# Performance work log

Hardware: AMD Instinct MI355X
Metric: run time of the kernel (lower is better)

The kernel has to match this reference:

```python
import jax, jax.numpy as jnp
import numpy as np

INPUT_DIM = 1024
HIDDEN_DIM = 1024


def setup_inputs() -> dict:
    key = jax.random.key(0)
    ks = jax.random.split(key, 7)
    B, S = 4, 2048
    s = 1.0 / np.sqrt(INPUT_DIM)
    x = jax.random.normal(ks[0], (B, S, INPUT_DIM), dtype=jnp.float32)
    Wq = jax.random.normal(ks[1], (HIDDEN_DIM, INPUT_DIM), dtype=jnp.float32) * s
    bq = jnp.zeros((HIDDEN_DIM,), dtype=jnp.float32)
    Wk = jax.random.normal(ks[2], (HIDDEN_DIM, INPUT_DIM), dtype=jnp.float32) * s
    bk = jnp.zeros((HIDDEN_DIM,), dtype=jnp.float32)
    Wv = jax.random.normal(ks[3], (HIDDEN_DIM, INPUT_DIM), dtype=jnp.float32) * s
    bv = jnp.zeros((HIDDEN_DIM,), dtype=jnp.float32)
    return {"x": x, "Wq": Wq, "bq": bq, "Wk": Wk, "bk": bk, "Wv": Wv, "bv": bv}


def reference(x, Wq, bq, Wk, bk, Wv, bv):
    # Linear layers: y = x @ W.T + b (torch nn.Linear convention)
    q = jnp.einsum('bsi,hi->bsh', x, Wq) + bq
    k = jnp.einsum('bsi,hi->bsh', x, Wk) + bk
    v = jnp.einsum('bsi,hi->bsh', x, Wv) + bv
    scale = 1.0 / jnp.sqrt(jnp.asarray(q.shape[-1], dtype=q.dtype))
    scores = jnp.einsum('bsh,bth->bst', q, k) * scale  # [B,S,S]
    attention_weights = jax.nn.softmax(scores, axis=-1)
    weighted_sum = jnp.einsum('bst,bth->bsh', attention_weights, v)
    return (weighted_sum, attention_weights)
```

## Files before the change

### kernel.cpp

```cpp
#include <hip/hip_runtime.h>
#include <hip/hip_bf16.h>
#include <cstdint>


typedef __bf16 bf16x8 __attribute__((ext_vector_type(8)));
typedef float  f32x4  __attribute__((ext_vector_type(4)));

__device__ __forceinline__ void load_lds16(const __bf16* g, __bf16* l) {
    __builtin_amdgcn_global_load_lds(
        (const __attribute__((address_space(1))) void*)g,
        (__attribute__((address_space(3))) void*)l,
        16, 0, 0);
}

__global__ __launch_bounds__(256) void cvt_f32_bf16(
        const float* __restrict__ src, __bf16* __restrict__ dst, int n8) {
    int i = blockIdx.x * blockDim.x + threadIdx.x;
    if (i >= n8) return;
    const float4* s4 = (const float4*)src;
    float4 a = s4[2 * i], b = s4[2 * i + 1];
    bf16x8 o;
    o[0] = (__bf16)a.x; o[1] = (__bf16)a.y; o[2] = (__bf16)a.z; o[3] = (__bf16)a.w;
    o[4] = (__bf16)b.x; o[5] = (__bf16)b.y; o[6] = (__bf16)b.z; o[7] = (__bf16)b.w;
    ((bf16x8*)dst)[i] = o;
}

__global__ __launch_bounds__(256) void pack_bias3(
        const float* __restrict__ a, const float* __restrict__ b,
        const float* __restrict__ c, float* __restrict__ o) {
    int i = blockIdx.x * blockDim.x + threadIdx.x;
    if (i < 1024) { o[i] = a[i]; o[i + 1024] = b[i]; o[i + 2048] = c[i]; }
}

template <int MODE>
__global__ __launch_bounds__(256, 3) void gemm_nt(
        const __bf16* __restrict__ A, const __bf16* __restrict__ Bt,
        void* __restrict__ C0, void* __restrict__ C1, void* __restrict__ C2,
        const float* __restrict__ bias,
        int lda, int ldb, int ldc, long sA, long sB, long sC,
        int K, float scale) {
    __shared__ __bf16 lA[128 * 64];
    __shared__ __bf16 lB[128 * 64];

    const int tid  = threadIdx.x;
    const int lane = tid & 63;
    const int wave = tid >> 6;
    const int mblk = blockIdx.y * 128;
    const int nblk = blockIdx.x * 128;
    const int z    = blockIdx.z;
    A  += (long)z * sA;
    Bt += (long)z * sB;

    const int wm = (wave >> 1) * 64;
    const int wn = (wave & 1) * 64;

    f32x4 zero = {0.f, 0.f, 0.f, 0.f};
    f32x4 acc[4][4];
#pragma unroll
    for (int i = 0; i < 4; ++i)
#pragma unroll
        for (int j = 0; j < 4; ++j) acc[i][j] = zero;

    const int rsel = lane & 15;
    const int quad = lane >> 4;

    int srow[4], scol[4];
#pragma unroll
    for (int it = 0; it < 4; ++it) {
        int s  = tid + it * 256;
        srow[it] = s >> 3;
        scol[it] = ((s & 7) ^ (srow[it] & 7)) * 8;
    }

    for (int k0 = 0; k0 < K; k0 += 64) {
#pragma unroll
        for (int it = 0; it < 4; ++it) {
            int s = tid + it * 256;
            load_lds16(A  + (long)(mblk + srow[it]) * lda + k0 + scol[it], lA + s * 8);
            load_lds16(Bt + (long)(nblk + srow[it]) * ldb + k0 + scol[it], lB + s * 8);
        }
        __syncthreads();

#pragma unroll
        for (int half = 0; half < 2; ++half) {
            const int cq = quad + half * 4;
            bf16x8 fa[4], fb[4];
#pragma unroll
            for (int i = 0; i < 4; ++i) {
                int ra = wm + i * 16 + rsel;
                fa[i] = *(const bf16x8*)&lA[(ra * 8 + (cq ^ (ra & 7))) * 8];
                int rb = wn + i * 16 + rsel;
                fb[i] = *(const bf16x8*)&lB[(rb * 8 + (cq ^ (rb & 7))) * 8];
            }
#pragma unroll
            for (int i = 0; i < 4; ++i)
#pragma unroll
                for (int j = 0; j < 4; ++j)
                    acc[i][j] = __builtin_amdgcn_mfma_f32_16x16x32_bf16(
                        fa[i], fb[j], acc[i][j], 0, 0, 0);
        }
        __syncthreads();
    }

    const int rq = quad * 4;
#pragma unroll
    for (int i = 0; i < 4; ++i) {
#pragma unroll
        for (int j = 0; j < 4; ++j) {
            const int n = nblk + wn + j * 16 + rsel;
            if constexpr (MODE == 0) {
                __bf16* C = (n < 1024) ? (__bf16*)C0
                          : (n < 2048) ? (__bf16*)C1 : (__bf16*)C2;
                const int col = n & 1023;
                float bv = bias[n];
#pragma unroll
                for (int r = 0; r < 4; ++r) {
                    int m = mblk + wm + i * 16 + rq + r;
                    C[(long)m * ldc + col] = (__bf16)(acc[i][j][r] + bv);
                }
            } else if constexpr (MODE == 1) {
                float* C = (float*)C0 + (long)z * sC;
#pragma unroll
                for (int r = 0; r < 4; ++r) {
                    int m = mblk + wm + i * 16 + rq + r;
                    C[(long)m * ldc + n] = acc[i][j][r] * scale;
                }
            } else {
                float* C = (float*)C0 + (long)z * sC;
#pragma unroll
                for (int r = 0; r < 4; ++r) {
                    int m = mblk + wm + i * 16 + rq + r;
                    C[(long)m * ldc + n] = acc[i][j][r];
                }
            }
        }
    }
}

__global__ __launch_bounds__(256) void softmax_rows(
        float* __restrict__ P, __bf16* __restrict__ Pb) {
    const long row = blockIdx.x;
    float*  p  = P  + row * 2048;
    __bf16* pb = Pb + row * 2048;
    const int tid  = threadIdx.x;
    const int lane = tid & 63;
    const int wave = tid >> 6;

    float4 v0 = ((const float4*)p)[tid * 2];
    float4 v1 = ((const float4*)p)[tid * 2 + 1];
    float e[8] = {v0.x, v0.y, v0.z, v0.w, v1.x, v1.y, v1.z, v1.w};

    float mx = e[0];
#pragma unroll
    for (int i = 1; i < 8; ++i) mx = fmaxf(mx, e[i]);
#pragma unroll
    for (int o = 1; o < 64; o <<= 1) mx = fmaxf(mx, __shfl_xor(mx, o, 64));

    __shared__ float redm[4], reds[4];
    if (lane == 0) redm[wave] = mx;
    __syncthreads();
    mx = fmaxf(fmaxf(redm[0], redm[1]), fmaxf(redm[2], redm[3]));

    float sum = 0.f;
#pragma unroll
    for (int i = 0; i < 8; ++i) { e[i] = __expf(e[i] - mx); sum += e[i]; }
#pragma unroll
    for (int o = 1; o < 64; o <<= 1) sum += __shfl_xor(sum, o, 64);
    if (lane == 0) reds[wave] = sum;
    __syncthreads();
    sum = reds[0] + reds[1] + reds[2] + reds[3];
    const float inv = 1.f / sum;

    float4 o0, o1;
    o0.x = e[0] * inv; o0.y = e[1] * inv; o0.z = e[2] * inv; o0.w = e[3] * inv;
    o1.x = e[4] * inv; o1.y = e[5] * inv; o1.z = e[6] * inv; o1.w = e[7] * inv;
    ((float4*)p)[tid * 2]     = o0;
    ((float4*)p)[tid * 2 + 1] = o1;
    bf16x8 ob;
    ob[0] = (__bf16)o0.x; ob[1] = (__bf16)o0.y; ob[2] = (__bf16)o0.z; ob[3] = (__bf16)o0.w;
    ob[4] = (__bf16)o1.x; ob[5] = (__bf16)o1.y; ob[6] = (__bf16)o1.z; ob[7] = (__bf16)o1.w;
    ((bf16x8*)pb)[tid] = ob;
}

__global__ __launch_bounds__(256) void transpose_v(
        const __bf16* __restrict__ src, __bf16* __restrict__ dst) {
    __shared__ __bf16 t[32][33];
    const int tx = threadIdx.x, ty = threadIdx.y;
    const int tileC = blockIdx.x * 32;
    const int tileR = blockIdx.y * 32;
    const long zs = (long)blockIdx.z * 2048 * 1024;
    const long zd = (long)blockIdx.z * 1024 * 2048;
#pragma unroll
    for (int k = 0; k < 4; ++k) {
        int r = ty * 4 + k;
        t[r][tx] = src[zs + (long)(tileR + r) * 1024 + tileC + tx];
    }
    __syncthreads();
#pragma unroll
    for (int k = 0; k < 4; ++k) {
        int c = ty * 4 + k;
        dst[zd + (long)(tileC + c) * 2048 + tileR + tx] = t[tx][c];
    }
}

extern "C" void kernel_launch(void* const* d_in, const int* in_sizes, int n_in,
                              void* d_out, int out_size, void* d_ws, size_t ws_size,
                              hipStream_t stream) {
    const float* x  = (const float*)d_in[0];
    const float* Wq = (const float*)d_in[1];
    const float* bq = (const float*)d_in[2];
    const float* Wk = (const float*)d_in[3];
    const float* bk = (const float*)d_in[4];
    const float* Wv = (const float*)d_in[5];
    const float* bv = (const float*)d_in[6];

    const int  S = 2048, H = 1024, I = 1024, B = 4;
    const long MS = (long)B * S;
    float* out_ws  = (float*)d_out;
    float* out_att = (float*)d_out + (long)B * S * H;

    char* w = (char*)d_ws;
    __bf16* x_bf   = (__bf16*)w; w += MS * I * 2;
    __bf16* wqkv   = (__bf16*)w; w += (long)3 * H * I * 2;
    float*  bias3  = (float*)w;  w += 4096 * 4;
    __bf16* q_bf   = (__bf16*)w; w += MS * H * 2;
    __bf16* k_bf   = (__bf16*)w; w += MS * H * 2;
    __bf16* v_bf   = (__bf16*)w; w += MS * H * 2;
    __bf16* vt_bf  = (__bf16*)w; w += MS * H * 2;
    __bf16* p_bf   = (__bf16*)w; w += (long)B * S * S * 2;

    {
        int n8 = (int)(MS * I / 8);
        cvt_f32_bf16<<<dim3((n8 + 255) / 256), dim3(256), 0, stream>>>(x, x_bf, n8);
        int w8 = H * I / 8;
        cvt_f32_bf16<<<dim3((w8 + 255) / 256), dim3(256), 0, stream>>>(Wq, wqkv, w8);
        cvt_f32_bf16<<<dim3((w8 + 255) / 256), dim3(256), 0, stream>>>(Wk, wqkv + (long)H * I, w8);
        cvt_f32_bf16<<<dim3((w8 + 255) / 256), dim3(256), 0, stream>>>(Wv, wqkv + (long)2 * H * I, w8);
        pack_bias3<<<dim3(4), dim3(256), 0, stream>>>(bq, bk, bv, bias3);
    }

    gemm_nt<0><<<dim3(24, 64, 1), dim3(256), 0, stream>>>(
        x_bf, wqkv, q_bf, k_bf, v_bf, bias3,
        1024, 1024, 1024, 0, 0, 0, 1024, 1.f);

    transpose_v<<<dim3(32, 64, 4), dim3(32, 8), 0, stream>>>(v_bf, vt_bf);

    gemm_nt<1><<<dim3(16, 16, 4), dim3(256), 0, stream>>>(
        q_bf, k_bf, out_att, nullptr, nullptr, nullptr,
        1024, 1024, 2048, (long)S * H, (long)S * H, (long)S * S, 1024, 0.03125f);

    softmax_rows<<<dim3(8192), dim3(256), 0, stream>>>(out_att, p_bf);

    gemm_nt<2><<<dim3(8, 16, 4), dim3(256), 0, stream>>>(
        p_bf, vt_bf, out_ws, nullptr, nullptr, nullptr,
        2048, 2048, 1024, (long)S * S, (long)S * H, (long)S * H, 2048, 1.f);
}
```

Baseline: 318.1 us.

## Fuse V transpose into QKV GEMM epilogue and merge conversion kernels

```diff
diff --git a/kernel.cpp b/kernel.cpp
--- a/kernel.cpp
+++ b/kernel.cpp
@@ -13,34 +13,52 @@
         16, 0, 0);
 }
 
-__global__ __launch_bounds__(256) void cvt_f32_bf16(
-        const float* __restrict__ src, __bf16* __restrict__ dst, int n8) {
-    int i = blockIdx.x * blockDim.x + threadIdx.x;
-    if (i >= n8) return;
+__global__ __launch_bounds__(256) void cvt_all(
+        const float* __restrict__ x,
+        const float* __restrict__ wq, const float* __restrict__ wk,
+        const float* __restrict__ wv,
+        const float* __restrict__ bq, const float* __restrict__ bk,
+        const float* __restrict__ bv,
+        __bf16* __restrict__ xb, __bf16* __restrict__ wb,
+        float* __restrict__ bias3) {
+    const long NX = 1048576, NW = 131072;
+    long i = (long)blockIdx.x * 256 + threadIdx.x;
+    const float* src; __bf16* dst; long c;
+    if (i < NX) { src = x; dst = xb; c = i; }
+    else if (i < NX + 3 * NW) {
+        long j = i - NX;
+        src = (j < NW) ? wq : (j < 2 * NW) ? wk : wv;
+        c = j % NW;
+        dst = wb + (j / NW) * (NW * 8);
+    } else if (i < NX + 3 * NW + 384) {
+        long cidx = i - (NX + 3 * NW);
+        int seg = (int)(cidx >> 7);
+        const float* bs = (seg == 0) ? bq : (seg == 1) ? bk : bv;
+        long off = (cidx & 127) * 8;
+        float4 a = *(const float4*)(bs + off);
+        float4 b = *(const float4*)(bs + off + 4);
+        *(float4*)(bias3 + cidx * 8)     = a;
+        *(float4*)(bias3 + cidx * 8 + 4) = b;
+        return;
+    } else return;
     const float4* s4 = (const float4*)src;
-    float4 a = s4[2 * i], b = s4[2 * i + 1];
+    float4 a = s4[2 * c], b = s4[2 * c + 1];
     bf16x8 o;
     o[0] = (__bf16)a.x; o[1] = (__bf16)a.y; o[2] = (__bf16)a.z; o[3] = (__bf16)a.w;
     o[4] = (__bf16)b.x; o[5] = (__bf16)b.y; o[6] = (__bf16)b.z; o[7] = (__bf16)b.w;
-    ((bf16x8*)dst)[i] = o;
-}
-
-__global__ __launch_bounds__(256) void pack_bias3(
-        const float* __restrict__ a, const float* __restrict__ b,
-        const float* __restrict__ c, float* __restrict__ o) {
-    int i = blockIdx.x * blockDim.x + threadIdx.x;
-    if (i < 1024) { o[i] = a[i]; o[i + 1024] = b[i]; o[i + 2048] = c[i]; }
+    ((bf16x8*)dst)[c] = o;
 }
 
 template <int MODE>
-__global__ __launch_bounds__(256, 3) void gemm_nt(
+__global__ __launch_bounds__(256, 4) void gemm_nt(
         const __bf16* __restrict__ A, const __bf16* __restrict__ Bt,
         void* __restrict__ C0, void* __restrict__ C1, void* __restrict__ C2,
         const float* __restrict__ bias,
         int lda, int ldb, int ldc, long sA, long sB, long sC,
         int K, float scale) {
-    __shared__ __bf16 lA[128 * 64];
-    __shared__ __bf16 lB[128 * 64];
+    __shared__ __bf16 smem[16384];
+    __bf16* lA = smem;
+    __bf16* lB = smem + 8192;
 
     const int tid  = threadIdx.x;
     const int lane = tid & 63;
@@ -103,34 +121,78 @@
     }
 
     const int rq = quad * 4;
-#pragma unroll
-    for (int i = 0; i < 4; ++i) {
-#pragma unroll
-        for (int j = 0; j < 4; ++j) {
-            const int n = nblk + wn + j * 16 + rsel;
-            if constexpr (MODE == 0) {
-                __bf16* C = (n < 1024) ? (__bf16*)C0
-                          : (n < 2048) ? (__bf16*)C1 : (__bf16*)C2;
-                const int col = n & 1023;
-                float bv = bias[n];
-#pragma unroll
-                for (int r = 0; r < 4; ++r) {
-                    int m = mblk + wm + i * 16 + rq + r;
-                    C[(long)m * ldc + col] = (__bf16)(acc[i][j][r] + bv);
-                }
-            } else if constexpr (MODE == 1) {
+    if constexpr (MODE == 0) {
+        if (nblk >= 2048) {
+            __bf16* tbuf = smem;
+#pragma unroll
+            for (int i = 0; i < 4; ++i) {
+#pragma unroll
+                for (int j = 0; j < 4; ++j) {
+                    const int n_loc = wn + j * 16 + rsel;
+                    const float bv = bias[nblk + n_loc];
+                    const int m_loc = wm + i * 16 + rq;
+                    const int c  = m_loc >> 3;
+                    const int cs = c ^ (n_loc & 15);
+                    __bf16* dst = &tbuf[n_loc * 128 + cs * 8 + (m_loc & 7)];
+                    __bf16 tmp[4];
+#pragma unroll
+                    for (int r = 0; r < 4; ++r) tmp[r] = (__bf16)(acc[i][j][r] + bv);
+                    *(uint64_t*)dst = *(const uint64_t*)tmp;
+                }
+            }
+            __syncthreads();
+            {
+                __bf16* vt = (__bf16*)C2;
+                const int n_loc = tid & 127;
+                const int cpart = tid >> 7;
+                const long b = mblk >> 11;
+                const long t0 = mblk & 2047;
+                const long h  = nblk - 2048 + n_loc;
+                __bf16* gdst = vt + b * (1024L * 2048) + h * 2048 + t0;
+#pragma unroll
+                for (int s = 0; s < 8; ++s) {
+                    int c  = cpart * 8 + s;
+                    int cs = c ^ (n_loc & 15);
+                    bf16x8 vchunk = *(const bf16x8*)&tbuf[n_loc * 128 + cs * 8];
+                    *(bf16x8*)(gdst + c * 8) = vchunk;
+                }
+            }
+        } else {
+#pragma unroll
+            for (int i = 0; i < 4; ++i) {
+#pragma unroll
+                for (int j = 0; j < 4; ++j) {
+                    const int n = nblk + wn + j * 16 + rsel;
+                    __bf16* C = (n < 1024) ? (__bf16*)C0 : (__bf16*)C1;
+                    const int col = n & 1023;
+                    float bv = bias[n];
+#pragma unroll
+                    for (int r = 0; r < 4; ++r) {
+                        int m = mblk + wm + i * 16 + rq + r;
+                        C[(long)m * ldc + col] = (__bf16)(acc[i][j][r] + bv);
+                    }
+                }
+            }
+        }
+    } else {
+#pragma unroll
+        for (int i = 0; i < 4; ++i) {
+#pragma unroll
+            for (int j = 0; j < 4; ++j) {
+                const int n = nblk + wn + j * 16 + rsel;
                 float* C = (float*)C0 + (long)z * sC;
-#pragma unroll
-                for (int r = 0; r < 4; ++r) {
-                    int m = mblk + wm + i * 16 + rq + r;
-                    C[(long)m * ldc + n] = acc[i][j][r] * scale;
-                }
-            } else {
-                float* C = (float*)C0 + (long)z * sC;
-#pragma unroll
-                for (int r = 0; r < 4; ++r) {
-                    int m = mblk + wm + i * 16 + rq + r;
-                    C[(long)m * ldc + n] = acc[i][j][r];
+                if constexpr (MODE == 1) {
+#pragma unroll
+                    for (int r = 0; r < 4; ++r) {
+                        int m = mblk + wm + i * 16 + rq + r;
+                        C[(long)m * ldc + n] = acc[i][j][r] * scale;
+                    }
+                } else {
+#pragma unroll
+                    for (int r = 0; r < 4; ++r) {
+                        int m = mblk + wm + i * 16 + rq + r;
+                        C[(long)m * ldc + n] = acc[i][j][r];
+                    }
                 }
             }
         }
@@ -180,27 +242,6 @@
     ob[0] = (__bf16)o0.x; ob[1] = (__bf16)o0.y; ob[2] = (__bf16)o0.z; ob[3] = (__bf16)o0.w;
     ob[4] = (__bf16)o1.x; ob[5] = (__bf16)o1.y; ob[6] = (__bf16)o1.z; ob[7] = (__bf16)o1.w;
     ((bf16x8*)pb)[tid] = ob;
-}
-
-__global__ __launch_bounds__(256) void transpose_v(
-        const __bf16* __restrict__ src, __bf16* __restrict__ dst) {
-    __shared__ __bf16 t[32][33];
-    const int tx = threadIdx.x, ty = threadIdx.y;
-    const int tileC = blockIdx.x * 32;
-    const int tileR = blockIdx.y * 32;
-    const long zs = (long)blockIdx.z * 2048 * 1024;
-    const long zd = (long)blockIdx.z * 1024 * 2048;
-#pragma unroll
-    for (int k = 0; k < 4; ++k) {
-        int r = ty * 4 + k;
-        t[r][tx] = src[zs + (long)(tileR + r) * 1024 + tileC + tx];
-    }
-    __syncthreads();
-#pragma unroll
-    for (int k = 0; k < 4; ++k) {
-        int c = ty * 4 + k;
-        dst[zd + (long)(tileC + c) * 2048 + tileR + tx] = t[tx][c];
-    }
 }
 
 extern "C" void kernel_launch(void* const* d_in, const int* in_sizes, int n_in,
@@ -225,25 +266,18 @@
     float*  bias3  = (float*)w;  w += 4096 * 4;
     __bf16* q_bf   = (__bf16*)w; w += MS * H * 2;
     __bf16* k_bf   = (__bf16*)w; w += MS * H * 2;
-    __bf16* v_bf   = (__bf16*)w; w += MS * H * 2;
     __bf16* vt_bf  = (__bf16*)w; w += MS * H * 2;
     __bf16* p_bf   = (__bf16*)w; w += (long)B * S * S * 2;
 
     {
-        int n8 = (int)(MS * I / 8);
-        cvt_f32_bf16<<<dim3((n8 + 255) / 256), dim3(256), 0, stream>>>(x, x_bf, n8);
-        int w8 = H * I / 8;
-        cvt_f32_bf16<<<dim3((w8 + 255) / 256), dim3(256), 0, stream>>>(Wq, wqkv, w8);
-        cvt_f32_bf16<<<dim3((w8 + 255) / 256), dim3(256), 0, stream>>>(Wk, wqkv + (long)H * I, w8);
-        cvt_f32_bf16<<<dim3((w8 + 255) / 256), dim3(256), 0, stream>>>(Wv, wqkv + (long)2 * H * I, w8);
-        pack_bias3<<<dim3(4), dim3(256), 0, stream>>>(bq, bk, bv, bias3);
+        long tot = 1048576 + 3 * 131072 + 384;
+        cvt_all<<<dim3((unsigned)((tot + 255) / 256)), dim3(256), 0, stream>>>(
+            x, Wq, Wk, Wv, bq, bk, bv, x_bf, wqkv, bias3);
     }
 
     gemm_nt<0><<<dim3(24, 64, 1), dim3(256), 0, stream>>>(
-        x_bf, wqkv, q_bf, k_bf, v_bf, bias3,
+        x_bf, wqkv, q_bf, k_bf, vt_bf, bias3,
         1024, 1024, 1024, 0, 0, 0, 1024, 1.f);
-
-    transpose_v<<<dim3(32, 64, 4), dim3(32, 8), 0, stream>>>(v_bf, vt_bf);
 
     gemm_nt<1><<<dim3(16, 16, 4), dim3(256), 0, stream>>>(
         q_bf, k_bf, out_att, nullptr, nullptr, nullptr,
```

New measurement: 299.0 us. -6.0%, faster.
